# Optimization experiments

Measured on AMD Instinct MI355X. Metric: run time of the kernel, lower is better.

Reference implementation:

```python
import jax, jax.numpy as jnp
import numpy as np

BATCH_SIZE = 4096
TEMPERATURE = 0.5
DIAG_NEG = -50000.0
EPS = 1e-8  # torch CosineSimilarity eps


def setup_inputs() -> dict:
    key = jax.random.key(0)
    k1, k2 = jax.random.split(key)
    z_i = jax.random.normal(k1, (BATCH_SIZE, 128), dtype=jnp.float32)
    z_j = jax.random.normal(k2, (BATCH_SIZE, 128), dtype=jnp.float32)
    return {"z_i": z_i, "z_j": z_j}


def reference(z_i, z_j):
    n = z_i.shape[0]
    z = jnp.concatenate([z_i, z_j], axis=0)  # [2N, D]
    # cosine similarity: normalize once, then one GEMM (same math as
    # CosineSimilarity(dim=2) on the broadcasted pair, with eps clamp on norms)
    norms = jnp.maximum(jnp.linalg.norm(z, axis=-1, keepdims=True), EPS)
    zn = z / norms
    sim = (zn @ zn.T) / TEMPERATURE  # [2N, 2N]
    # mask self-similarity on the diagonal
    idx = jnp.arange(2 * n)
    sim = sim.at[idx, idx].set(DIAG_NEG)
    # labels: positive pair is the other view
    labels = jnp.concatenate([idx[n:], idx[:n]])  # [2N]
    # mean softmax cross-entropy
    logp = jax.nn.log_softmax(sim, axis=-1)
    loss = -jnp.mean(logp[idx, labels])
    return loss
```

## Files before the change

kernel.cpp:

```cpp
#include <hip/hip_runtime.h>

#define N2 8192
#define NHALF 4096
#define DDIM 128
#define NCHUNK 16
#define CPC 512
#define NT 8
#define LN2F 0.69314718055994530942f
#define SCALEF 1.6986436f

typedef __attribute__((ext_vector_type(8))) short bf8_t;
typedef __attribute__((ext_vector_type(4))) float f4_t;

__device__ __forceinline__ float fexp2(float x) { return __builtin_amdgcn_exp2f(x); }
__device__ __forceinline__ float flog2(float x) { return __builtin_amdgcn_logf(x); }

__device__ __forceinline__ unsigned short f2bf(float f) {
  unsigned int x = __float_as_uint(f);
  x += 0x7fffu + ((x >> 16) & 1u);
  return (unsigned short)(x >> 16);
}

__global__ __launch_bounds__(256) void knorm(const float* __restrict__ zi,
                                             const float* __restrict__ zj,
                                             unsigned short* __restrict__ u) {
  const int lane = threadIdx.x & 63;
  const int w = threadIdx.x >> 6;
  const int half = lane >> 5;
  const int l32 = lane & 31;
  const int row = blockIdx.x * 8 + w * 2 + half;
  const float* src = (row < NHALF) ? (zi + (size_t)row * DDIM)
                                   : (zj + (size_t)(row - NHALF) * DDIM);
  float4 x = *(const float4*)(src + l32 * 4);
  float ss = x.x * x.x + x.y * x.y + x.z * x.z + x.w * x.w;
#pragma unroll
  for (int m = 16; m; m >>= 1) ss += __shfl_xor(ss, m);
  const float scale = SCALEF / fmaxf(sqrtf(ss), 1e-8f);
  const unsigned int p0 = (unsigned int)f2bf(x.x * scale) |
                          ((unsigned int)f2bf(x.y * scale) << 16);
  const unsigned int p1 = (unsigned int)f2bf(x.z * scale) |
                          ((unsigned int)f2bf(x.w * scale) << 16);
  uint2 pk; pk.x = p0; pk.y = p1;
  *(uint2*)(u + (size_t)row * DDIM + l32 * 4) = pk;
}

__global__ __launch_bounds__(512) void ksim(const unsigned short* __restrict__ u,
                                            float* __restrict__ Lp) {
  __shared__ short Bls[32768];
  const int tid = threadIdx.x;
  const int lane = tid & 63;
  const int w = tid >> 6;
  const int rb = blockIdx.x >> 4;
  const int chunk = blockIdx.x & 15;
  const int lr = lane & 15, lq = lane >> 4;
  const int rowbase = rb * 256;
  const int colbase = chunk * CPC;

#pragma unroll
  for (int i = 0; i < 8; i++) {
    const int k = w * 8 + i;
    const int row_local = k * 4 + lq;
    const int sdu = lr ^ (4 * (k & 1) + lq);
    const unsigned short* src =
        u + (size_t)(rowbase + row_local) * DDIM + sdu * 8;
    short* dst = &Bls[k * 512];
    __builtin_amdgcn_global_load_lds(
        (const __attribute__((address_space(1))) unsigned int*)src,
        (__attribute__((address_space(3))) unsigned int*)dst, 16, 0, 0);
  }
  asm volatile("s_waitcnt vmcnt(0)" ::: "memory");
  __builtin_amdgcn_sched_barrier(0);
  __builtin_amdgcn_s_barrier();
  __builtin_amdgcn_sched_barrier(0);

  bf8_t a[2][4];
#pragma unroll
  for (int s = 0; s < 2; s++)
#pragma unroll
    for (int kc = 0; kc < 4; kc++) {
      const int R = w * 32 + s * 16 + lr;
      a[s][kc] = *(const bf8_t*)&Bls[(R * 16 + ((kc * 4 + lq) ^ (lr & 7))) * 8];
    }
#pragma unroll
  for (int s = 0; s < 2; s++)
#pragma unroll
    for (int kc = 0; kc < 4; kc++)
      asm volatile("" : "+v"(a[s][kc]));
  __builtin_amdgcn_sched_barrier(0);
  __builtin_amdgcn_s_barrier();
  __builtin_amdgcn_sched_barrier(0);

  f4_t L0 = {0.f, 0.f, 0.f, 0.f}, L1 = {0.f, 0.f, 0.f, 0.f};

  auto STAGE = [&](int t) {
#pragma unroll
    for (int i = 0; i < 2; i++) {
      const int j = w * 2 + i;
      const int col_local = j * 4 + lq;
      const int sdu = lr ^ (4 * (j & 1) + lq);
      const unsigned short* src =
          u + (size_t)(colbase + t * 64 + col_local) * DDIM + sdu * 8;
      short* dst = &Bls[(t % 3) * 8192 + j * 512];
      __builtin_amdgcn_global_load_lds(
          (const __attribute__((address_space(1))) unsigned int*)src,
          (__attribute__((address_space(3))) unsigned int*)dst, 16, 0, 0);
    }
  };

  auto COMP = [&](int t) {
    const short* P = &Bls[(t % 3) * 8192];
#pragma unroll
    for (int g = 0; g < 4; g++) {
      bf8_t bv[4];
#pragma unroll
      for (int kc = 0; kc < 4; kc++)
        bv[kc] = *(const bf8_t*)&P[((g * 16 + lr) * 16 +
                                    ((kc * 4 + lq) ^ (lr & 7))) * 8];
      f4_t acc0 = {0.f, 0.f, 0.f, 0.f}, acc1 = {0.f, 0.f, 0.f, 0.f};
#pragma unroll
      for (int kc = 0; kc < 4; kc++) {
        acc0 = __builtin_amdgcn_mfma_f32_16x16x32_bf16(a[0][kc], bv[kc], acc0, 0, 0, 0);
        acc1 = __builtin_amdgcn_mfma_f32_16x16x32_bf16(a[1][kc], bv[kc], acc1, 0, 0, 0);
      }
#pragma unroll
      for (int r = 0; r < 4; r++) {
        L0[r] += fexp2(acc0[r]);
        L1[r] += fexp2(acc1[r]);
      }
    }
  };

  STAGE(0);
  STAGE(1);
#pragma unroll 1
  for (int t = 0; t < NT; ++t) {
    if (t < NT - 1) {
      asm volatile("s_waitcnt vmcnt(2)" ::: "memory");
    } else {
      asm volatile("s_waitcnt vmcnt(0)" ::: "memory");
    }
    __builtin_amdgcn_sched_barrier(0);
    __builtin_amdgcn_s_barrier();
    __builtin_amdgcn_sched_barrier(0);
    COMP(t);
    if (t + 2 < NT) STAGE(t + 2);
  }

#pragma unroll
  for (int r = 0; r < 4; r++) {
    float v0 = L0[r], v1 = L1[r];
    v0 += __shfl_xor(v0, 1); v0 += __shfl_xor(v0, 2);
    v0 += __shfl_xor(v0, 4); v0 += __shfl_xor(v0, 8);
    v1 += __shfl_xor(v1, 1); v1 += __shfl_xor(v1, 2);
    v1 += __shfl_xor(v1, 4); v1 += __shfl_xor(v1, 8);
    if (lr == 0) {
      const int rrow = rowbase + w * 32 + lq * 4 + r;
      Lp[(size_t)rrow * NCHUNK + chunk] = v0;
      Lp[(size_t)(rrow + 16) * NCHUNK + chunk] = v1;
    }
  }
}

__global__ __launch_bounds__(256) void krow(const unsigned short* __restrict__ u,
                                            const float* __restrict__ Lp,
                                            float* __restrict__ bsum) {
  const int lane = threadIdx.x & 63;
  const int w = threadIdx.x >> 6;
  const int i = blockIdx.x * 4 + w;
  const int j = (i + NHALF) & (N2 - 1);

  const unsigned int av = ((const unsigned int*)(u + (size_t)i * DDIM))[lane];
  const unsigned int bv = ((const unsigned int*)(u + (size_t)j * DDIM))[lane];
  const float f0 = __uint_as_float(av << 16);
  const float f1 = __uint_as_float(av & 0xffff0000u);
  const float g0 = __uint_as_float(bv << 16);
  const float g1 = __uint_as_float(bv & 0xffff0000u);
  float dot = f0 * g0 + f1 * g1;
  float dd = f0 * f0 + f1 * f1;
  float ls = (lane < NCHUNK) ? Lp[(size_t)i * NCHUNK + lane] : 0.f;
#pragma unroll
  for (int m = 32; m; m >>= 1) {
    dot += __shfl_xor(dot, m);
    dd += __shfl_xor(dd, m);
    ls += __shfl_xor(ls, m);
  }
  __shared__ float sred[4];
  if (lane == 0) {
    const float L = ls - fexp2(dd);
    sred[w] = LN2F * (flog2(L) - dot);
  }
  __syncthreads();
  if (threadIdx.x == 0)
    bsum[blockIdx.x] = sred[0] + sred[1] + sred[2] + sred[3];
}

__global__ void kfinal(const float* __restrict__ bsum, float* __restrict__ out) {
  float v = 0.f;
#pragma unroll
  for (int jj = 0; jj < 32; jj++) v += bsum[threadIdx.x + 64 * jj];
#pragma unroll
  for (int m = 32; m; m >>= 1) v += __shfl_xor(v, m);
  if (threadIdx.x == 0) out[0] = v * (1.0f / N2);
}

extern "C" void kernel_launch(void* const* d_in, const int* in_sizes, int n_in,
                              void* d_out, int out_size, void* d_ws, size_t ws_size,
                              hipStream_t stream) {
  const float* zi = (const float*)d_in[0];
  const float* zj = (const float*)d_in[1];
  char* ws = (char*)d_ws;
  unsigned short* u = (unsigned short*)ws;
  float* Lp = (float*)(ws + (size_t)N2 * DDIM * 2);
  float* bsum = (float*)(ws + (size_t)N2 * DDIM * 2 + (size_t)NCHUNK * N2 * 4);
  float* out = (float*)d_out;

  hipLaunchKernelGGL(knorm, dim3(N2 / 8), dim3(256), 0, stream, zi, zj, u);
  hipLaunchKernelGGL(ksim, dim3((N2 / 256) * NCHUNK), dim3(512), 0, stream, u, Lp);
  hipLaunchKernelGGL(krow, dim3(N2 / 4), dim3(256), 0, stream, u, Lp, bsum);
  hipLaunchKernelGGL(kfinal, dim3(1), dim3(64), 0, stream, bsum, out);
}
```

Baseline: 35.17 us.

## Exploit similarity matrix symmetry by computing only upper-triangular tiles

The similarity kernel now runs only over upper-triangular 256x256 tile pairs (I<=J). Each off-diagonal tile adds its exp sums both per row (into slot J) and per column, the column sums gathered through shared memory and written into slot I. This roughly halves the MFMA and exp work. In exchange it adds shuffles, a shared-memory column reduction, a while loop to decode the tile index, and a larger partial-sum buffer that krow reads with 32 lanes.

```diff
diff --git a/kernel.cpp b/kernel.cpp
--- a/kernel.cpp
+++ b/kernel.cpp
@@ -3,9 +3,9 @@
 #define N2 8192
 #define NHALF 4096
 #define DDIM 128
-#define NCHUNK 16
-#define CPC 512
-#define NT 8
+#define NB 32
+#define NSLOT 32
+#define NT 4
 #define LN2F 0.69314718055994530942f
 #define SCALEF 1.6986436f
 
@@ -47,14 +47,17 @@
 __global__ __launch_bounds__(512) void ksim(const unsigned short* __restrict__ u,
                                             float* __restrict__ Lp) {
   __shared__ short Bls[32768];
+  __shared__ float CSl[8][256];
   const int tid = threadIdx.x;
   const int lane = tid & 63;
   const int w = tid >> 6;
-  const int rb = blockIdx.x >> 4;
-  const int chunk = blockIdx.x & 15;
+  int bres = blockIdx.x, I = 0;
+  while (bres >= NB - I) { bres -= NB - I; I++; }
+  const int J = I + bres;
+  const bool offdiag = (J > I);
   const int lr = lane & 15, lq = lane >> 4;
-  const int rowbase = rb * 256;
-  const int colbase = chunk * CPC;
+  const int rowbase = I * 256;
+  const int colbase = J * 256;
 
 #pragma unroll
   for (int i = 0; i < 8; i++) {
@@ -122,10 +125,18 @@
         acc0 = __builtin_amdgcn_mfma_f32_16x16x32_bf16(a[0][kc], bv[kc], acc0, 0, 0, 0);
         acc1 = __builtin_amdgcn_mfma_f32_16x16x32_bf16(a[1][kc], bv[kc], acc1, 0, 0, 0);
       }
+      float s8 = 0.f;
 #pragma unroll
       for (int r = 0; r < 4; r++) {
-        L0[r] += fexp2(acc0[r]);
-        L1[r] += fexp2(acc1[r]);
+        const float e0 = fexp2(acc0[r]);
+        const float e1 = fexp2(acc1[r]);
+        L0[r] += e0; L1[r] += e1;
+        s8 += e0 + e1;
+      }
+      if (offdiag) {
+        s8 += __shfl_xor(s8, 16);
+        s8 += __shfl_xor(s8, 32);
+        if (lq == 0) CSl[w][t * 64 + g * 16 + lr] = s8;
       }
     }
   };
@@ -155,8 +166,17 @@
     v1 += __shfl_xor(v1, 4); v1 += __shfl_xor(v1, 8);
     if (lr == 0) {
       const int rrow = rowbase + w * 32 + lq * 4 + r;
-      Lp[(size_t)rrow * NCHUNK + chunk] = v0;
-      Lp[(size_t)(rrow + 16) * NCHUNK + chunk] = v1;
+      Lp[(size_t)rrow * NSLOT + J] = v0;
+      Lp[(size_t)(rrow + 16) * NSLOT + J] = v1;
+    }
+  }
+  if (offdiag) {
+    __syncthreads();
+    if (tid < 256) {
+      float cs = 0.f;
+#pragma unroll
+      for (int k = 0; k < 8; k++) cs += CSl[k][tid];
+      Lp[(size_t)(colbase + tid) * NSLOT + I] = cs;
     }
   }
 }
@@ -177,7 +197,7 @@
   const float g1 = __uint_as_float(bv & 0xffff0000u);
   float dot = f0 * g0 + f1 * g1;
   float dd = f0 * f0 + f1 * f1;
-  float ls = (lane < NCHUNK) ? Lp[(size_t)i * NCHUNK + lane] : 0.f;
+  float ls = (lane < NSLOT) ? Lp[(size_t)i * NSLOT + lane] : 0.f;
 #pragma unroll
   for (int m = 32; m; m >>= 1) {
     dot += __shfl_xor(dot, m);
@@ -211,11 +231,11 @@
   char* ws = (char*)d_ws;
   unsigned short* u = (unsigned short*)ws;
   float* Lp = (float*)(ws + (size_t)N2 * DDIM * 2);
-  float* bsum = (float*)(ws + (size_t)N2 * DDIM * 2 + (size_t)NCHUNK * N2 * 4);
+  float* bsum = (float*)(ws + (size_t)N2 * DDIM * 2 + (size_t)NSLOT * N2 * 4);
   float* out = (float*)d_out;
 
   hipLaunchKernelGGL(knorm, dim3(N2 / 8), dim3(256), 0, stream, zi, zj, u);
-  hipLaunchKernelGGL(ksim, dim3((N2 / 256) * NCHUNK), dim3(512), 0, stream, u, Lp);
+  hipLaunchKernelGGL(ksim, dim3(NB * (NB + 1) / 2), dim3(512), 0, stream, u, Lp);
   hipLaunchKernelGGL(krow, dim3(N2 / 4), dim3(256), 0, stream, u, Lp, bsum);
   hipLaunchKernelGGL(kfinal, dim3(1), dim3(64), 0, stream, bsum, out);
 }
```

Result: slower. 36.80 us (+4.6%).
